# Kernel tuning notes

Measured on AMD Instinct MI355X. Metric: run time of the kernel, lower is better.

Reference implementation:

```python
import jax, jax.numpy as jnp
import numpy as np

B, N, R, E = 4, 50000, 100000, 1_600_000   # batch, nodes (wavelets_col), wavelets_row, nnz
D_IN, H1, H2, D_OUT = 32, 32, 16, 1
NEG_SLOPE = 0.2


def _xavier(k, shape):
    lim = float(np.sqrt(6.0 / (shape[0] + shape[1])))
    return jax.random.uniform(k, shape, jnp.float32, -lim, lim)


def setup_inputs() -> dict:
    key = jax.random.key(0)
    ks = jax.random.split(key, 16)
    # wavelets: sparse (R x N); inverse wavelets: sparse (N x R)
    w_rows = jax.random.randint(ks[0], (E,), 0, R)
    w_cols = jax.random.randint(ks[1], (E,), 0, N)
    wi_rows = jax.random.randint(ks[2], (E,), 0, N)
    wi_cols = jax.random.randint(ks[3], (E,), 0, R)
    return {
        "wavelets_indices": jnp.stack([w_rows, w_cols]),
        "wavelets_values": jax.random.normal(ks[4], (E,), jnp.float32) * 0.05,
        "wavelets_inverse_indices": jnp.stack([wi_rows, wi_cols]),
        "wavelets_inverse_values": jax.random.normal(ks[5], (E,), jnp.float32) * 0.05,
        "x_features": jax.random.normal(ks[6], (B, N, D_IN), jnp.float32),
        "W1": _xavier(ks[7], (D_IN, H1)),
        "diag1": 0.9 + 0.2 * jax.random.uniform(ks[8], (R,), jnp.float32),
        "W2": _xavier(ks[9], (H1, H2)),
        "diag2": 0.9 + 0.2 * jax.random.uniform(ks[10], (R,), jnp.float32),
        "reg_co_w": _xavier(ks[11], (H2, D_OUT)),
        "reg_co_b": jnp.zeros((D_OUT,), jnp.float32),
        "reg_co2_w": _xavier(ks[12], (H2, D_OUT)),
        "reg_co2_b": jnp.zeros((D_OUT,), jnp.float32),
    }


def _gw_layer(x, W, diag, w_idx, w_val, wi_idx, wi_val):
    # filtered = X @ W  -> (B, N, d)
    h = jnp.einsum("bnd,de->bne", x, W)
    d = W.shape[1]
    # T = wavelets (R x N) @ h  : scatter-add of gathered edge messages
    msg = h[:, w_idx[1], :] * w_val[None, :, None]          # (B, E, d)
    t = jnp.zeros((x.shape[0], R, d), h.dtype).at[:, w_idx[0], :].add(msg)
    # out = (wavelets_inverse * diag) (N x R) @ T  (diag rescales columns)
    coef = wi_val * diag[wi_idx[1]]                         # (E,)
    msg2 = t[:, wi_idx[1], :] * coef[None, :, None]         # (B, E, d)
    out = jnp.zeros((x.shape[0], N, d), h.dtype).at[:, wi_idx[0], :].add(msg2)
    return jax.nn.leaky_relu(out, NEG_SLOPE)                # dropout p=0.0 -> identity


def reference(wavelets_indices, wavelets_values, wavelets_inverse_indices,
              wavelets_inverse_values, x_features, W1, diag1, W2, diag2,
              reg_co_w, reg_co_b, reg_co2_w, reg_co2_b):
    x = _gw_layer(x_features, W1, diag1, wavelets_indices, wavelets_values,
                  wavelets_inverse_indices, wavelets_inverse_values)
    x = _gw_layer(x, W2, diag2, wavelets_indices, wavelets_values,
                  wavelets_inverse_indices, wavelets_inverse_values)
    co = x[:, -2, :] @ reg_co_w + reg_co_b                  # (B, 1)
    co2 = x[:, -1, :] @ reg_co2_w + reg_co2_b               # (B, 1)
    return jnp.concatenate([co[:, None, :], co2[:, None, :]], axis=1)  # (B, 2, 1)
```

## Files before the change

kernel.cpp:

```cpp
#include <hip/hip_runtime.h>

#define NEG_SLOPE 0.2f

static const int B = 4, N = 50000, R = 100000, E = 1600000;
static const int X2_CAP = 4096;
static const int R2_CAP = 4096;
static const int N1_CAP = 4096;
static const int WDEG  = 64;
static const int WIDEG = 96;
static const int RBW = 3200;
static const int NBW = 1600;


__global__ void fusedA(const float* __restrict__ x, const float* __restrict__ W1,
                       float* __restrict__ h1,
                       const int4* __restrict__ wi_rows4, const int* __restrict__ wi_cols,
                       const float* __restrict__ wi_val,
                       unsigned* __restrict__ bitsR1, int2* __restrict__ x2list,
                       int* __restrict__ x2tail, int* __restrict__ r2list,
                       int* __restrict__ r2tail, int e4, int G1) {
    if ((int)blockIdx.x < G1) {
        __shared__ float sW[32 * 32];
        for (int i = threadIdx.x; i < 1024; i += blockDim.x) sW[i] = W1[i];
        __syncthreads();
        int id = blockIdx.x * blockDim.x + threadIdx.x;
        if (id >= N * B) return;
        int n = id >> 2, b = id & 3;
        const float* xr = x + ((size_t)b * N + n) * 32;
        float acc[32];
#pragma unroll
        for (int c = 0; c < 32; ++c) acc[c] = 0.f;
#pragma unroll
        for (int k = 0; k < 32; ++k) {
            float xv = xr[k];
#pragma unroll
            for (int c = 0; c < 32; ++c) acc[c] += xv * sW[k * 32 + c];
        }
        float* o = h1 + ((size_t)n * B + b) * 32;
#pragma unroll
        for (int c = 0; c < 32; ++c) o[c] = acc[c];
    } else {
        int blk = blockIdx.x - G1;
        int base = blk * (blockDim.x * 4) + threadIdx.x;
#pragma unroll
        for (int k = 0; k < 4; ++k) {
            int i = base + k * blockDim.x;
            if (i >= e4) continue;
            int4 r = wi_rows4[i];
            int rr[4] = {r.x, r.y, r.z, r.w};
#pragma unroll
            for (int j = 0; j < 4; ++j) {
                if (rr[j] >= N - 2) {
                    int ed = i * 4 + j;
                    int col = wi_cols[ed];
                    unsigned old = atomicOr(&bitsR1[col >> 5], 1u << (col & 31));
                    if (!((old >> (col & 31)) & 1u)) {
                        int p = atomicAdd(r2tail, 1);
                        if (p < R2_CAP) r2list[p] = col;
                    }
                    int pos = atomicAdd(x2tail, 1);
                    if (pos < X2_CAP)
                        x2list[pos] = make_int2(col * 2 + (rr[j] - (N - 2)),
                                                __float_as_int(wi_val[ed]));
                }
            }
        }
    }
}

__global__ void markB(const int4* __restrict__ w_rows4, const int* __restrict__ w_cols,
                      const unsigned* __restrict__ bitsR1, unsigned* __restrict__ bitsN1,
                      int* __restrict__ n1list, int* __restrict__ n1slot,
                      int* __restrict__ n1tail, int e4) {
    __shared__ int lcount, gbase;
    __shared__ int sbuf[1024];
    if (threadIdx.x == 0) lcount = 0;
    __syncthreads();
    int lane = threadIdx.x & 63;
    int i = blockIdx.x * blockDim.x + threadIdx.x;
    int4 r = make_int4(-1, -1, -1, -1);
    if (i < e4) r = w_rows4[i];
    int rr[4] = {r.x, r.y, r.z, r.w};
    unsigned fb[4];
#pragma unroll
    for (int j = 0; j < 4; ++j)
        fb[j] = (rr[j] >= 0) ? ((bitsR1[rr[j] >> 5] >> (rr[j] & 31)) & 1u) : 0u;
#pragma unroll
    for (int j = 0; j < 4; ++j) {
        bool isnew = false;
        int c = 0;
        if (fb[j]) {
            c = w_cols[i * 4 + j];
            unsigned old = atomicOr(&bitsN1[c >> 5], 1u << (c & 31));
            isnew = ((old >> (c & 31)) & 1u) == 0u;
        }
        unsigned long long m = __ballot(isnew);
        if (m) {
            int leader = __ffsll(m) - 1;
            int b0 = 0;
            if (lane == leader) b0 = atomicAdd(&lcount, __popcll(m));
            b0 = __shfl(b0, leader);
            if (isnew) sbuf[b0 + __popcll(m & ((1ull << lane) - 1))] = c;
        }
    }
    __syncthreads();
    if (threadIdx.x == 0) gbase = atomicAdd(n1tail, lcount);
    __syncthreads();
    for (int t = threadIdx.x; t < lcount; t += blockDim.x) {
        int n = sbuf[t];
        int slot = gbase + t;
        n1list[slot] = n;
        n1slot[n] = slot;
    }
}

__global__ void markC_wi(const int4* __restrict__ wi_rows4, const int* __restrict__ wi_cols,
                         const float* __restrict__ wi_val, const float* __restrict__ diag1,
                         const unsigned* __restrict__ bitsN1, const int* __restrict__ n1slot,
                         unsigned* __restrict__ bitsR2, int* __restrict__ wi_cnt,
                         int2* __restrict__ wi_pairsD,
                         int* __restrict__ r1list, int* __restrict__ r1tail, int e4) {
    __shared__ int lcount2, gbase2;
    __shared__ int r1buf[1024];
    if (threadIdx.x == 0) lcount2 = 0;
    __syncthreads();
    int lane = threadIdx.x & 63;
    int i = blockIdx.x * blockDim.x + threadIdx.x;
    int4 r = make_int4(-1, -1, -1, -1);
    if (i < e4) r = wi_rows4[i];
    int rr[4] = {r.x, r.y, r.z, r.w};
    unsigned fb[4];
#pragma unroll
    for (int j = 0; j < 4; ++j)
        fb[j] = (rr[j] >= 0) ? ((bitsN1[rr[j] >> 5] >> (rr[j] & 31)) & 1u) : 0u;
#pragma unroll
    for (int j = 0; j < 4; ++j) {
        bool isnew = false;
        int col = 0;
        if (fb[j]) {
            int ed = i * 4 + j;
            col = wi_cols[ed];
            float cf = wi_val[ed] * diag1[col];
            int slot = n1slot[rr[j]];
            int pos = atomicAdd(&wi_cnt[rr[j]], 1);
            if (slot < N1_CAP && pos < WIDEG)
                wi_pairsD[(size_t)slot * WIDEG + pos] =
                    make_int2(col, __float_as_int(cf));
            unsigned old = atomicOr(&bitsR2[col >> 5], 1u << (col & 31));
            isnew = ((old >> (col & 31)) & 1u) == 0u;
        }
        unsigned long long m2 = __ballot(isnew);
        if (m2) {
            int leader = __ffsll(m2) - 1;
            int b0 = 0;
            if (lane == leader) b0 = atomicAdd(&lcount2, __popcll(m2));
            b0 = __shfl(b0, leader);
            if (isnew)
                r1buf[b0 + __popcll(m2 & ((1ull << lane) - 1))] = col;
        }
    }
    __syncthreads();
    if (threadIdx.x == 0) gbase2 = atomicAdd(r1tail, lcount2);
    __syncthreads();
    for (int t = threadIdx.x; t < lcount2; t += blockDim.x) r1list[gbase2 + t] = r1buf[t];
}

__global__ void wplace(const int4* __restrict__ w_rows4, const int4* __restrict__ w_cols4,
                       const float4* __restrict__ w_val4,
                       const unsigned* __restrict__ bitsR1, const unsigned* __restrict__ bitsR2,
                       int* __restrict__ w_cnt, int2* __restrict__ w_pairsD, int e4) {
    int i = blockIdx.x * blockDim.x + threadIdx.x;
    if (i >= e4) return;
    int4 r = w_rows4[i];
    int4 c = w_cols4[i];
    float4 v = w_val4[i];
    int rr[4] = {r.x, r.y, r.z, r.w};
    int cc[4] = {c.x, c.y, c.z, c.w};
    float vv[4] = {v.x, v.y, v.z, v.w};
    unsigned fl[4];
#pragma unroll
    for (int j = 0; j < 4; ++j)
        fl[j] = ((bitsR1[rr[j] >> 5] | bitsR2[rr[j] >> 5]) >> (rr[j] & 31)) & 1u;
#pragma unroll
    for (int j = 0; j < 4; ++j) {
        if (fl[j]) {
            int pos = atomicAdd(&w_cnt[rr[j]], 1);
            if (pos < WDEG)
                w_pairsD[(size_t)rr[j] * WDEG + pos] =
                    make_int2(cc[j], __float_as_int(vv[j]));
        }
    }
}

__global__ void gather_t1(const float* __restrict__ h1, float* __restrict__ t1,
                          const int* __restrict__ w_cnt, const int2* __restrict__ w_pairsD,
                          const int* __restrict__ r1list, const int* __restrict__ r1tail) {
    int total = (*r1tail) * 32;
    int gstride = gridDim.x * blockDim.x;
    for (int idx = blockIdx.x * blockDim.x + threadIdx.x; idx < total; idx += gstride) {
        int row = r1list[idx >> 5];
        int rem = idx & 31;
        int c4 = rem & 7;
        int b = rem >> 3;
        int L = w_cnt[row]; if (L > WDEG) L = WDEG;
        const int2* pr = w_pairsD + (size_t)row * WDEG;
        const float4* sb = (const float4*)h1 + b * 8 + c4;
        float4 acc = make_float4(0.f, 0.f, 0.f, 0.f);
        int i = 0;
        int L4 = L & ~3;
        for (; i < L4; i += 4) {
            int2 p0 = pr[i + 0];
            int2 p1 = pr[i + 1];
            int2 p2 = pr[i + 2];
            int2 p3 = pr[i + 3];
            float4 s0 = sb[(size_t)p0.x * 32];
            float4 s1 = sb[(size_t)p1.x * 32];
            float4 s2 = sb[(size_t)p2.x * 32];
            float4 s3 = sb[(size_t)p3.x * 32];
            float v0 = __int_as_float(p0.y), v1 = __int_as_float(p1.y);
            float v2 = __int_as_float(p2.y), v3 = __int_as_float(p3.y);
            acc.x += v0 * s0.x + v1 * s1.x + v2 * s2.x + v3 * s3.x;
            acc.y += v0 * s0.y + v1 * s1.y + v2 * s2.y + v3 * s3.y;
            acc.z += v0 * s0.z + v1 * s1.z + v2 * s2.z + v3 * s3.z;
            acc.w += v0 * s0.w + v1 * s1.w + v2 * s2.w + v3 * s3.w;
        }
        for (; i < L; ++i) {
            int2 p = pr[i];
            float4 sv = sb[(size_t)p.x * 32];
            float v = __int_as_float(p.y);
            acc.x += v * sv.x; acc.y += v * sv.y; acc.z += v * sv.z; acc.w += v * sv.w;
        }
        ((float4*)t1)[(size_t)row * 32 + b * 8 + c4] = acc;
    }
}

__global__ void x1gemm2(const float* __restrict__ t1, const float* __restrict__ W2,
                        float* __restrict__ h2,
                        const int* __restrict__ n1list, const int* __restrict__ wi_cnt,
                        const int2* __restrict__ wi_pairsD,
                        const int* __restrict__ n1tail) {
    __shared__ float sW[32 * 16];
    __shared__ float xls[8][128];
    for (int i = threadIdx.x; i < 512; i += blockDim.x) sW[i] = W2[i];
    int n1c = *n1tail; if (n1c > N1_CAP) n1c = N1_CAP;
    int g = threadIdx.x >> 5;
    int t32 = threadIdx.x & 31;
    int b = t32 >> 3, c4 = t32 & 7;
    for (int base = blockIdx.x * 8; base < n1c; base += gridDim.x * 8) {
        int s = base + g;
        bool active = (s < n1c);
        int n = 0;
        if (active) {
            n = n1list[s];
            int L = wi_cnt[n]; if (L > WIDEG) L = WIDEG;
            const int2* pr = wi_pairsD + (size_t)s * WIDEG;
            const float4* sb = (const float4*)t1 + b * 8 + c4;
            float4 acc = make_float4(0.f, 0.f, 0.f, 0.f);
            int i = 0;
            int L2 = L & ~1;
            for (; i < L2; i += 2) {
                int2 p0 = pr[i + 0];
                int2 p1 = pr[i + 1];
                float4 s0 = sb[(size_t)p0.x * 32];
                float4 s1 = sb[(size_t)p1.x * 32];
                float v0 = __int_as_float(p0.y), v1 = __int_as_float(p1.y);
                acc.x += v0 * s0.x + v1 * s1.x;
                acc.y += v0 * s0.y + v1 * s1.y;
                acc.z += v0 * s0.z + v1 * s1.z;
                acc.w += v0 * s0.w + v1 * s1.w;
            }
            if (i < L) {
                int2 p = pr[i];
                float4 sv = sb[(size_t)p.x * 32];
                float v = __int_as_float(p.y);
                acc.x += v * sv.x; acc.y += v * sv.y; acc.z += v * sv.z; acc.w += v * sv.w;
            }
            float* xp = &xls[g][b * 32 + c4 * 4];
            xp[0] = acc.x > 0.f ? acc.x : NEG_SLOPE * acc.x;
            xp[1] = acc.y > 0.f ? acc.y : NEG_SLOPE * acc.y;
            xp[2] = acc.z > 0.f ? acc.z : NEG_SLOPE * acc.z;
            xp[3] = acc.w > 0.f ? acc.w : NEG_SLOPE * acc.w;
        }
        __syncthreads();
        if (active) {
#pragma unroll
            for (int half = 0; half < 2; ++half) {
                int o = t32 + half * 32;
                int bb = o >> 4, cc = o & 15;
                const float* xp = &xls[g][bb * 32];
                float acc = 0.f;
#pragma unroll
                for (int k = 0; k < 32; ++k) acc += xp[k] * sW[k * 16 + cc];
                h2[(size_t)n * 64 + o] = acc;
            }
        }
        __syncthreads();
    }
}

__global__ void t2x2heads(const float* __restrict__ h2,
                          const int* __restrict__ w_cnt, const int2* __restrict__ w_pairsD,
                          const int* __restrict__ r2list, const int* __restrict__ r2tail,
                          float* __restrict__ t2,
                          const int2* __restrict__ x2list, const int* __restrict__ x2tail,
                          const float* __restrict__ diag2,
                          const float* __restrict__ rw1, const float* __restrict__ rb1,
                          const float* __restrict__ rw2, const float* __restrict__ rb2,
                          float* __restrict__ out) {
    int r2c = *r2tail; if (r2c > R2_CAP) r2c = R2_CAP;
    for (int idx = threadIdx.x; idx < r2c * 16; idx += blockDim.x) {
        int row = r2list[idx >> 4];
        int rem = idx & 15;
        int c4 = rem & 3;
        int b = rem >> 2;
        int L = w_cnt[row]; if (L > WDEG) L = WDEG;
        const int2* pr = w_pairsD + (size_t)row * WDEG;
        const float4* sb = (const float4*)h2 + b * 4 + c4;
        float4 acc = make_float4(0.f, 0.f, 0.f, 0.f);
        for (int i = 0; i < L; ++i) {
            int2 p = pr[i];
            float4 sv = sb[(size_t)p.x * 16];
            float v = __int_as_float(p.y);
            acc.x += v * sv.x; acc.y += v * sv.y; acc.z += v * sv.z; acc.w += v * sv.w;
        }
        ((float4*)t2)[(size_t)row * 16 + b * 4 + c4] = acc;
    }
    __syncthreads();

    int cnt = *x2tail; if (cnt > X2_CAP) cnt = X2_CAP;
    int g = threadIdx.x >> 6, l = threadIdx.x & 63;
    int b = l >> 4, c = l & 15;
    float a0 = 0.f, a1 = 0.f;
    for (int i = g; i < cnt; i += 16) {
        int2 rec = x2list[i];
        int col = rec.x >> 1;
        float coef = __int_as_float(rec.y) * diag2[col];
        float v = t2[(size_t)col * 64 + b * 16 + c] * coef;
        if (rec.x & 1) a1 += v; else a0 += v;
    }
    __shared__ float red0[16][64], red1[16][64], xs[2][64];
    red0[g][l] = a0; red1[g][l] = a1;
    __syncthreads();
    if (threadIdx.x < 64) {
        float s0 = 0.f, s1 = 0.f;
#pragma unroll
        for (int gg = 0; gg < 16; ++gg) { s0 += red0[gg][l]; s1 += red1[gg][l]; }
        xs[0][l] = s0; xs[1][l] = s1;
    }
    __syncthreads();
    if (threadIdx.x < 8) {
        int bb = threadIdx.x >> 1, which = threadIdx.x & 1;
        const float* w = which ? rw2 : rw1;
        float acc = which ? rb2[0] : rb1[0];
        for (int k = 0; k < 16; ++k) {
            float xv = xs[which][bb * 16 + k];
            xv = xv > 0.f ? xv : NEG_SLOPE * xv;
            acc += xv * w[k];
        }
        out[bb * 2 + which] = acc;
    }
}

extern "C" void kernel_launch(void* const* d_in, const int* in_sizes, int n_in,
                              void* d_out, int out_size, void* d_ws, size_t ws_size,
                              hipStream_t stream) {
    const int*   w_rows  = (const int*)d_in[0];
    const int*   w_cols  = ((const int*)d_in[0]) + E;
    const float* w_val   = (const float*)d_in[1];
    const int*   wi_rows = (const int*)d_in[2];
    const int*   wi_cols = ((const int*)d_in[2]) + E;
    const float* wi_val  = (const float*)d_in[3];
    const float* x       = (const float*)d_in[4];
    const float* W1      = (const float*)d_in[5];
    const float* diag1   = (const float*)d_in[6];
    const float* W2      = (const float*)d_in[7];
    const float* diag2   = (const float*)d_in[8];
    const float* rw1     = (const float*)d_in[9];
    const float* rb1     = (const float*)d_in[10];
    const float* rw2     = (const float*)d_in[11];
    const float* rb2     = (const float*)d_in[12];
    float* out = (float*)d_out;

    float* h1 = (float*)d_ws;
    float* t1 = h1 + (size_t)B * N * 32;
    float* h2 = t1 + (size_t)B * R * 32;
    int* ip = (int*)(h2 + (size_t)B * N * 16);
    int* w_cnt  = ip; ip += R;
    int* wi_cnt = ip; ip += N;
    unsigned* bitsR1 = (unsigned*)ip; ip += RBW;
    unsigned* bitsR2 = (unsigned*)ip; ip += RBW;
    unsigned* bitsN1 = (unsigned*)ip; ip += NBW;
    int* tails  = ip; ip += 8;
    size_t zero_words = (size_t)(ip - w_cnt);
    int*  n1slot = ip; ip += N;
    int*  n1list = ip; ip += N;
    int*  r1list = ip; ip += R;
    int*  r2list = ip; ip += R2_CAP;
    int2* x2list = (int2*)ip; ip += 2 * X2_CAP;
    int2* w_pairsD  = (int2*)ip; ip += 2 * (size_t)R * WDEG;
    int2* wi_pairsD = (int2*)ip; ip += 2 * (size_t)N1_CAP * WIDEG;

    float* t2 = t1;

    const int blk = 256;
    const int e4 = E / 4;
    const int G1 = (N * B + blk - 1) / blk;
    const int G2 = (e4 + blk * 4 - 1) / (blk * 4);
    const int scanGrid = (e4 + blk - 1) / blk;

    (void)hipMemsetAsync(w_cnt, 0, zero_words * sizeof(int), stream);

    fusedA<<<G1 + G2, blk, 0, stream>>>(x, W1, h1, (const int4*)wi_rows, wi_cols, wi_val,
                                        bitsR1, x2list, tails + 0, r2list, tails + 1,
                                        e4, G1);
    markB<<<scanGrid, blk, 0, stream>>>((const int4*)w_rows, w_cols, bitsR1, bitsN1,
                                        n1list, n1slot, tails + 2, e4);
    markC_wi<<<scanGrid, blk, 0, stream>>>((const int4*)wi_rows, wi_cols, wi_val, diag1,
                                           bitsN1, n1slot, bitsR2, wi_cnt, wi_pairsD,
                                           r1list, tails + 3, e4);
    wplace<<<scanGrid, blk, 0, stream>>>((const int4*)w_rows, (const int4*)w_cols,
                                         (const float4*)w_val, bitsR1, bitsR2,
                                         w_cnt, w_pairsD, e4);
    gather_t1<<<4096, blk, 0, stream>>>(h1, t1, w_cnt, w_pairsD, r1list, tails + 3);
    x1gemm2<<<256, blk, 0, stream>>>(t1, W2, h2, n1list, wi_cnt, wi_pairsD, tails + 2);
    t2x2heads<<<1, 1024, 0, stream>>>(h2, w_cnt, w_pairsD, r2list, tails + 1,
                                      t2, x2list, tails + 0, diag2,
                                      rw1, rb1, rw2, rb2, out);
}
```

Measured before the change: 278.1 us.

## Build full CSR for both matrices and fuse layer-1 into per-node gather MLP

Replaces the multi-pass marking pipeline (fusedA/markB/markC_wi/wplace/gather_t1/x1gemm2) with a single build kernel that buckets every edge of both sparse matrices by row, a small kernel that derives the needed node set from the final rows, and a fused kernel. The fused kernel aggregates raw x through the two sparse hops, then applies W1, leaky ReLU and W2 per needed node. It relies on linearity to move the W1 projection after aggregation, so no full h1 or t1 is materialized. In exchange it writes full bucket lists for all edges with unconditional atomics and recomputes the inner t rows per (node, edge).

```diff
diff --git a/kernel.cpp b/kernel.cpp
--- a/kernel.cpp
+++ b/kernel.cpp
@@ -10,289 +10,170 @@
 static const int WIDEG = 96;
 static const int RBW = 3200;
 static const int NBW = 1600;
-
-
-__global__ void fusedA(const float* __restrict__ x, const float* __restrict__ W1,
-                       float* __restrict__ h1,
-                       const int4* __restrict__ wi_rows4, const int* __restrict__ wi_cols,
-                       const float* __restrict__ wi_val,
-                       unsigned* __restrict__ bitsR1, int2* __restrict__ x2list,
-                       int* __restrict__ x2tail, int* __restrict__ r2list,
-                       int* __restrict__ r2tail, int e4, int G1) {
-    if ((int)blockIdx.x < G1) {
-        __shared__ float sW[32 * 32];
-        for (int i = threadIdx.x; i < 1024; i += blockDim.x) sW[i] = W1[i];
-        __syncthreads();
-        int id = blockIdx.x * blockDim.x + threadIdx.x;
-        if (id >= N * B) return;
-        int n = id >> 2, b = id & 3;
-        const float* xr = x + ((size_t)b * N + n) * 32;
-        float acc[32];
-#pragma unroll
-        for (int c = 0; c < 32; ++c) acc[c] = 0.f;
-#pragma unroll
-        for (int k = 0; k < 32; ++k) {
-            float xv = xr[k];
-#pragma unroll
-            for (int c = 0; c < 32; ++c) acc[c] += xv * sW[k * 32 + c];
-        }
-        float* o = h1 + ((size_t)n * B + b) * 32;
-#pragma unroll
-        for (int c = 0; c < 32; ++c) o[c] = acc[c];
-    } else {
-        int blk = blockIdx.x - G1;
-        int base = blk * (blockDim.x * 4) + threadIdx.x;
-#pragma unroll
-        for (int k = 0; k < 4; ++k) {
-            int i = base + k * blockDim.x;
-            if (i >= e4) continue;
-            int4 r = wi_rows4[i];
-            int rr[4] = {r.x, r.y, r.z, r.w};
-#pragma unroll
-            for (int j = 0; j < 4; ++j) {
-                if (rr[j] >= N - 2) {
-                    int ed = i * 4 + j;
-                    int col = wi_cols[ed];
-                    unsigned old = atomicOr(&bitsR1[col >> 5], 1u << (col & 31));
-                    if (!((old >> (col & 31)) & 1u)) {
-                        int p = atomicAdd(r2tail, 1);
-                        if (p < R2_CAP) r2list[p] = col;
-                    }
-                    int pos = atomicAdd(x2tail, 1);
-                    if (pos < X2_CAP)
-                        x2list[pos] = make_int2(col * 2 + (rr[j] - (N - 2)),
-                                                __float_as_int(wi_val[ed]));
+static const int ZWORDS = R + N + RBW + NBW + 8;
+
+
+__global__ void buildK(const int4* __restrict__ w_rows4, const int4* __restrict__ w_cols4,
+                       const float4* __restrict__ w_val4,
+                       const int4* __restrict__ wi_rows4, const int4* __restrict__ wi_cols4,
+                       const float4* __restrict__ wi_val4,
+                       int* __restrict__ w_cnt, int2* __restrict__ w_pairsD,
+                       int* __restrict__ wi_cnt, int2* __restrict__ wi_pairsD,
+                       unsigned* __restrict__ bitsR2d, int* __restrict__ r2list,
+                       int2* __restrict__ x2list, int* __restrict__ tails, int e4) {
+    int i = blockIdx.x * blockDim.x + threadIdx.x;
+    if (i < e4) {
+        int4 r = w_rows4[i];
+        int4 c = w_cols4[i];
+        float4 v = w_val4[i];
+        int rr[4] = {r.x, r.y, r.z, r.w};
+        int cc[4] = {c.x, c.y, c.z, c.w};
+        float vv[4] = {v.x, v.y, v.z, v.w};
+        int pos[4];
+#pragma unroll
+        for (int j = 0; j < 4; ++j) pos[j] = atomicAdd(&w_cnt[rr[j]], 1);
+#pragma unroll
+        for (int j = 0; j < 4; ++j)
+            if (pos[j] < WDEG)
+                w_pairsD[(size_t)rr[j] * WDEG + pos[j]] =
+                    make_int2(cc[j], __float_as_int(vv[j]));
+    } else if (i < 2 * e4) {
+        int k = i - e4;
+        int4 r = wi_rows4[k];
+        int4 c = wi_cols4[k];
+        float4 v = wi_val4[k];
+        int rr[4] = {r.x, r.y, r.z, r.w};
+        int cc[4] = {c.x, c.y, c.z, c.w};
+        float vv[4] = {v.x, v.y, v.z, v.w};
+        int pos[4];
+#pragma unroll
+        for (int j = 0; j < 4; ++j) pos[j] = atomicAdd(&wi_cnt[rr[j]], 1);
+#pragma unroll
+        for (int j = 0; j < 4; ++j)
+            if (pos[j] < WIDEG)
+                wi_pairsD[(size_t)rr[j] * WIDEG + pos[j]] =
+                    make_int2(cc[j], __float_as_int(vv[j]));
+#pragma unroll
+        for (int j = 0; j < 4; ++j) {
+            if (rr[j] >= N - 2) {
+                int col = cc[j];
+                unsigned old = atomicOr(&bitsR2d[col >> 5], 1u << (col & 31));
+                if (!((old >> (col & 31)) & 1u)) {
+                    int p = atomicAdd(&tails[1], 1);
+                    if (p < R2_CAP) r2list[p] = col;
                 }
-            }
-        }
-    }
-}
-
-__global__ void markB(const int4* __restrict__ w_rows4, const int* __restrict__ w_cols,
-                      const unsigned* __restrict__ bitsR1, unsigned* __restrict__ bitsN1,
-                      int* __restrict__ n1list, int* __restrict__ n1slot,
-                      int* __restrict__ n1tail, int e4) {
-    __shared__ int lcount, gbase;
-    __shared__ int sbuf[1024];
-    if (threadIdx.x == 0) lcount = 0;
-    __syncthreads();
-    int lane = threadIdx.x & 63;
-    int i = blockIdx.x * blockDim.x + threadIdx.x;
-    int4 r = make_int4(-1, -1, -1, -1);
-    if (i < e4) r = w_rows4[i];
-    int rr[4] = {r.x, r.y, r.z, r.w};
-    unsigned fb[4];
-#pragma unroll
-    for (int j = 0; j < 4; ++j)
-        fb[j] = (rr[j] >= 0) ? ((bitsR1[rr[j] >> 5] >> (rr[j] & 31)) & 1u) : 0u;
-#pragma unroll
-    for (int j = 0; j < 4; ++j) {
-        bool isnew = false;
-        int c = 0;
-        if (fb[j]) {
-            c = w_cols[i * 4 + j];
+                int q = atomicAdd(&tails[0], 1);
+                if (q < X2_CAP)
+                    x2list[q] = make_int2(col * 2 + (rr[j] - (N - 2)),
+                                          __float_as_int(vv[j]));
+            }
+        }
+    }
+}
+
+__global__ void n1build(const int* __restrict__ r2list,
+                        const int* __restrict__ w_cnt, const int2* __restrict__ w_pairsD,
+                        unsigned* __restrict__ bitsN1, int* __restrict__ n1list,
+                        int* __restrict__ tails) {
+    int r2c = tails[1]; if (r2c > R2_CAP) r2c = R2_CAP;
+    int total = r2c * WDEG;
+    for (int item = threadIdx.x; item < total; item += blockDim.x) {
+        int ri = item >> 6;
+        int e  = item & 63;
+        int row = r2list[ri];
+        int L = w_cnt[row]; if (L > WDEG) L = WDEG;
+        if (e < L) {
+            int c = w_pairsD[(size_t)row * WDEG + e].x;
             unsigned old = atomicOr(&bitsN1[c >> 5], 1u << (c & 31));
-            isnew = ((old >> (c & 31)) & 1u) == 0u;
-        }
-        unsigned long long m = __ballot(isnew);
-        if (m) {
-            int leader = __ffsll(m) - 1;
-            int b0 = 0;
-            if (lane == leader) b0 = atomicAdd(&lcount, __popcll(m));
-            b0 = __shfl(b0, leader);
-            if (isnew) sbuf[b0 + __popcll(m & ((1ull << lane) - 1))] = c;
-        }
-    }
-    __syncthreads();
-    if (threadIdx.x == 0) gbase = atomicAdd(n1tail, lcount);
-    __syncthreads();
-    for (int t = threadIdx.x; t < lcount; t += blockDim.x) {
-        int n = sbuf[t];
-        int slot = gbase + t;
-        n1list[slot] = n;
-        n1slot[n] = slot;
-    }
-}
-
-__global__ void markC_wi(const int4* __restrict__ wi_rows4, const int* __restrict__ wi_cols,
-                         const float* __restrict__ wi_val, const float* __restrict__ diag1,
-                         const unsigned* __restrict__ bitsN1, const int* __restrict__ n1slot,
-                         unsigned* __restrict__ bitsR2, int* __restrict__ wi_cnt,
-                         int2* __restrict__ wi_pairsD,
-                         int* __restrict__ r1list, int* __restrict__ r1tail, int e4) {
-    __shared__ int lcount2, gbase2;
-    __shared__ int r1buf[1024];
-    if (threadIdx.x == 0) lcount2 = 0;
-    __syncthreads();
-    int lane = threadIdx.x & 63;
-    int i = blockIdx.x * blockDim.x + threadIdx.x;
-    int4 r = make_int4(-1, -1, -1, -1);
-    if (i < e4) r = wi_rows4[i];
-    int rr[4] = {r.x, r.y, r.z, r.w};
-    unsigned fb[4];
-#pragma unroll
-    for (int j = 0; j < 4; ++j)
-        fb[j] = (rr[j] >= 0) ? ((bitsN1[rr[j] >> 5] >> (rr[j] & 31)) & 1u) : 0u;
-#pragma unroll
-    for (int j = 0; j < 4; ++j) {
-        bool isnew = false;
-        int col = 0;
-        if (fb[j]) {
-            int ed = i * 4 + j;
-            col = wi_cols[ed];
-            float cf = wi_val[ed] * diag1[col];
-            int slot = n1slot[rr[j]];
-            int pos = atomicAdd(&wi_cnt[rr[j]], 1);
-            if (slot < N1_CAP && pos < WIDEG)
-                wi_pairsD[(size_t)slot * WIDEG + pos] =
-                    make_int2(col, __float_as_int(cf));
-            unsigned old = atomicOr(&bitsR2[col >> 5], 1u << (col & 31));
-            isnew = ((old >> (col & 31)) & 1u) == 0u;
-        }
-        unsigned long long m2 = __ballot(isnew);
-        if (m2) {
-            int leader = __ffsll(m2) - 1;
-            int b0 = 0;
-            if (lane == leader) b0 = atomicAdd(&lcount2, __popcll(m2));
-            b0 = __shfl(b0, leader);
-            if (isnew)
-                r1buf[b0 + __popcll(m2 & ((1ull << lane) - 1))] = col;
-        }
-    }
-    __syncthreads();
-    if (threadIdx.x == 0) gbase2 = atomicAdd(r1tail, lcount2);
-    __syncthreads();
-    for (int t = threadIdx.x; t < lcount2; t += blockDim.x) r1list[gbase2 + t] = r1buf[t];
-}
-
-__global__ void wplace(const int4* __restrict__ w_rows4, const int4* __restrict__ w_cols4,
-                       const float4* __restrict__ w_val4,
-                       const unsigned* __restrict__ bitsR1, const unsigned* __restrict__ bitsR2,
-                       int* __restrict__ w_cnt, int2* __restrict__ w_pairsD, int e4) {
-    int i = blockIdx.x * blockDim.x + threadIdx.x;
-    if (i >= e4) return;
-    int4 r = w_rows4[i];
-    int4 c = w_cols4[i];
-    float4 v = w_val4[i];
-    int rr[4] = {r.x, r.y, r.z, r.w};
-    int cc[4] = {c.x, c.y, c.z, c.w};
-    float vv[4] = {v.x, v.y, v.z, v.w};
-    unsigned fl[4];
-#pragma unroll
-    for (int j = 0; j < 4; ++j)
-        fl[j] = ((bitsR1[rr[j] >> 5] | bitsR2[rr[j] >> 5]) >> (rr[j] & 31)) & 1u;
-#pragma unroll
-    for (int j = 0; j < 4; ++j) {
-        if (fl[j]) {
-            int pos = atomicAdd(&w_cnt[rr[j]], 1);
-            if (pos < WDEG)
-                w_pairsD[(size_t)rr[j] * WDEG + pos] =
-                    make_int2(cc[j], __float_as_int(vv[j]));
-        }
-    }
-}
-
-__global__ void gather_t1(const float* __restrict__ h1, float* __restrict__ t1,
-                          const int* __restrict__ w_cnt, const int2* __restrict__ w_pairsD,
-                          const int* __restrict__ r1list, const int* __restrict__ r1tail) {
-    int total = (*r1tail) * 32;
-    int gstride = gridDim.x * blockDim.x;
-    for (int idx = blockIdx.x * blockDim.x + threadIdx.x; idx < total; idx += gstride) {
-        int row = r1list[idx >> 5];
-        int rem = idx & 31;
-        int c4 = rem & 7;
-        int b = rem >> 3;
-        int L = w_cnt[row]; if (L > WDEG) L = WDEG;
-        const int2* pr = w_pairsD + (size_t)row * WDEG;
-        const float4* sb = (const float4*)h1 + b * 8 + c4;
+            if (!((old >> (c & 31)) & 1u)) {
+                int p = atomicAdd(&tails[2], 1);
+                if (p < N1_CAP) n1list[p] = c;
+            }
+        }
+    }
+}
+
+__global__ void __launch_bounds__(256) x1mlp(
+        const float* __restrict__ x, const float* __restrict__ diag1,
+        const float* __restrict__ W1, const float* __restrict__ W2,
+        const int* __restrict__ n1list, const int* __restrict__ tails,
+        const int* __restrict__ wi_cnt, const int2* __restrict__ wi_pairsD,
+        const int* __restrict__ w_cnt, const int2* __restrict__ w_pairsD,
+        float* __restrict__ h2) {
+    __shared__ float W1s[1024], W2s[512];
+    __shared__ float uls[8][128];
+    __shared__ float ufin[128], x1ls[128];
+    for (int i = threadIdx.x; i < 1024; i += 256) W1s[i] = W1[i];
+    for (int i = threadIdx.x; i < 512; i += 256) W2s[i] = W2[i];
+    int n1c = tails[2]; if (n1c > N1_CAP) n1c = N1_CAP;
+    int g = threadIdx.x >> 5, t32 = threadIdx.x & 31;
+    int b = t32 >> 3, c4 = t32 & 7;
+    const float4* xb = (const float4*)x + (size_t)b * N * 8 + c4;
+    for (int s = blockIdx.x; s < n1c; s += gridDim.x) {
+        int n = n1list[s];
+        int L = wi_cnt[n]; if (L > WIDEG) L = WIDEG;
+        const int2* wip = wi_pairsD + (size_t)n * WIDEG;
         float4 acc = make_float4(0.f, 0.f, 0.f, 0.f);
-        int i = 0;
-        int L4 = L & ~3;
-        for (; i < L4; i += 4) {
-            int2 p0 = pr[i + 0];
-            int2 p1 = pr[i + 1];
-            int2 p2 = pr[i + 2];
-            int2 p3 = pr[i + 3];
-            float4 s0 = sb[(size_t)p0.x * 32];
-            float4 s1 = sb[(size_t)p1.x * 32];
-            float4 s2 = sb[(size_t)p2.x * 32];
-            float4 s3 = sb[(size_t)p3.x * 32];
-            float v0 = __int_as_float(p0.y), v1 = __int_as_float(p1.y);
-            float v2 = __int_as_float(p2.y), v3 = __int_as_float(p3.y);
-            acc.x += v0 * s0.x + v1 * s1.x + v2 * s2.x + v3 * s3.x;
-            acc.y += v0 * s0.y + v1 * s1.y + v2 * s2.y + v3 * s3.y;
-            acc.z += v0 * s0.z + v1 * s1.z + v2 * s2.z + v3 * s3.z;
-            acc.w += v0 * s0.w + v1 * s1.w + v2 * s2.w + v3 * s3.w;
-        }
-        for (; i < L; ++i) {
-            int2 p = pr[i];
-            float4 sv = sb[(size_t)p.x * 32];
-            float v = __int_as_float(p.y);
-            acc.x += v * sv.x; acc.y += v * sv.y; acc.z += v * sv.z; acc.w += v * sv.w;
-        }
-        ((float4*)t1)[(size_t)row * 32 + b * 8 + c4] = acc;
-    }
-}
-
-__global__ void x1gemm2(const float* __restrict__ t1, const float* __restrict__ W2,
-                        float* __restrict__ h2,
-                        const int* __restrict__ n1list, const int* __restrict__ wi_cnt,
-                        const int2* __restrict__ wi_pairsD,
-                        const int* __restrict__ n1tail) {
-    __shared__ float sW[32 * 16];
-    __shared__ float xls[8][128];
-    for (int i = threadIdx.x; i < 512; i += blockDim.x) sW[i] = W2[i];
-    int n1c = *n1tail; if (n1c > N1_CAP) n1c = N1_CAP;
-    int g = threadIdx.x >> 5;
-    int t32 = threadIdx.x & 31;
-    int b = t32 >> 3, c4 = t32 & 7;
-    for (int base = blockIdx.x * 8; base < n1c; base += gridDim.x * 8) {
-        int s = base + g;
-        bool active = (s < n1c);
-        int n = 0;
-        if (active) {
-            n = n1list[s];
-            int L = wi_cnt[n]; if (L > WIDEG) L = WIDEG;
-            const int2* pr = wi_pairsD + (size_t)s * WIDEG;
-            const float4* sb = (const float4*)t1 + b * 8 + c4;
-            float4 acc = make_float4(0.f, 0.f, 0.f, 0.f);
+        for (int e = g; e < L; e += 8) {
+            int2 pe = wip[e];
+            int r = pe.x;
+            float coef = __int_as_float(pe.y) * diag1[r];
+            int Lw = w_cnt[r]; if (Lw > WDEG) Lw = WDEG;
+            const int2* pr = w_pairsD + (size_t)r * WDEG;
+            float4 t = make_float4(0.f, 0.f, 0.f, 0.f);
             int i = 0;
-            int L2 = L & ~1;
-            for (; i < L2; i += 2) {
+            int L4 = Lw & ~3;
+            for (; i < L4; i += 4) {
                 int2 p0 = pr[i + 0];
                 int2 p1 = pr[i + 1];
-                float4 s0 = sb[(size_t)p0.x * 32];
-                float4 s1 = sb[(size_t)p1.x * 32];
+                int2 p2 = pr[i + 2];
+                int2 p3 = pr[i + 3];
+                float4 s0 = xb[(size_t)p0.x * 8];
+                float4 s1 = xb[(size_t)p1.x * 8];
+                float4 s2 = xb[(size_t)p2.x * 8];
+                float4 s3 = xb[(size_t)p3.x * 8];
                 float v0 = __int_as_float(p0.y), v1 = __int_as_float(p1.y);
-                acc.x += v0 * s0.x + v1 * s1.x;
-                acc.y += v0 * s0.y + v1 * s1.y;
-                acc.z += v0 * s0.z + v1 * s1.z;
-                acc.w += v0 * s0.w + v1 * s1.w;
-            }
-            if (i < L) {
+                float v2 = __int_as_float(p2.y), v3 = __int_as_float(p3.y);
+                t.x += v0 * s0.x + v1 * s1.x + v2 * s2.x + v3 * s3.x;
+                t.y += v0 * s0.y + v1 * s1.y + v2 * s2.y + v3 * s3.y;
+                t.z += v0 * s0.z + v1 * s1.z + v2 * s2.z + v3 * s3.z;
+                t.w += v0 * s0.w + v1 * s1.w + v2 * s2.w + v3 * s3.w;
+            }
+            for (; i < Lw; ++i) {
                 int2 p = pr[i];
-                float4 sv = sb[(size_t)p.x * 32];
+                float4 sv = xb[(size_t)p.x * 8];
                 float v = __int_as_float(p.y);
-                acc.x += v * sv.x; acc.y += v * sv.y; acc.z += v * sv.z; acc.w += v * sv.w;
-            }
-            float* xp = &xls[g][b * 32 + c4 * 4];
-            xp[0] = acc.x > 0.f ? acc.x : NEG_SLOPE * acc.x;
-            xp[1] = acc.y > 0.f ? acc.y : NEG_SLOPE * acc.y;
-            xp[2] = acc.z > 0.f ? acc.z : NEG_SLOPE * acc.z;
-            xp[3] = acc.w > 0.f ? acc.w : NEG_SLOPE * acc.w;
-        }
-        __syncthreads();
-        if (active) {
-#pragma unroll
-            for (int half = 0; half < 2; ++half) {
-                int o = t32 + half * 32;
-                int bb = o >> 4, cc = o & 15;
-                const float* xp = &xls[g][bb * 32];
-                float acc = 0.f;
-#pragma unroll
-                for (int k = 0; k < 32; ++k) acc += xp[k] * sW[k * 16 + cc];
-                h2[(size_t)n * 64 + o] = acc;
-            }
+                t.x += v * sv.x; t.y += v * sv.y; t.z += v * sv.z; t.w += v * sv.w;
+            }
+            acc.x += coef * t.x; acc.y += coef * t.y;
+            acc.z += coef * t.z; acc.w += coef * t.w;
+        }
+        float* up = &uls[g][b * 32 + c4 * 4];
+        up[0] = acc.x; up[1] = acc.y; up[2] = acc.z; up[3] = acc.w;
+        __syncthreads();
+        if (threadIdx.x < 128) {
+            float sum = 0.f;
+#pragma unroll
+            for (int gg = 0; gg < 8; ++gg) sum += uls[gg][threadIdx.x];
+            ufin[threadIdx.x] = sum;
+        }
+        __syncthreads();
+        if (threadIdx.x < 128) {
+            int bb = threadIdx.x >> 5, c = threadIdx.x & 31;
+            const float* ur = &ufin[bb * 32];
+            float o = 0.f;
+#pragma unroll
+            for (int k = 0; k < 32; ++k) o += ur[k] * W1s[k * 32 + c];
+            x1ls[threadIdx.x] = o > 0.f ? o : NEG_SLOPE * o;
+        }
+        __syncthreads();
+        if (threadIdx.x < 64) {
+            int bb = threadIdx.x >> 4, c = threadIdx.x & 15;
+            const float* xr = &x1ls[bb * 32];
+            float o = 0.f;
+#pragma unroll
+            for (int k = 0; k < 32; ++k) o += xr[k] * W2s[k * 16 + c];
+            h2[(size_t)n * 64 + bb * 16 + c] = o;
         }
         __syncthreads();
     }
@@ -300,14 +181,14 @@
 
 __global__ void t2x2heads(const float* __restrict__ h2,
                           const int* __restrict__ w_cnt, const int2* __restrict__ w_pairsD,
-                          const int* __restrict__ r2list, const int* __restrict__ r2tail,
+                          const int* __restrict__ r2list, const int* __restrict__ tails,
                           float* __restrict__ t2,
-                          const int2* __restrict__ x2list, const int* __restrict__ x2tail,
+                          const int2* __restrict__ x2list,
                           const float* __restrict__ diag2,
                           const float* __restrict__ rw1, const float* __restrict__ rb1,
                           const float* __restrict__ rw2, const float* __restrict__ rb2,
                           float* __restrict__ out) {
-    int r2c = *r2tail; if (r2c > R2_CAP) r2c = R2_CAP;
+    int r2c = tails[1]; if (r2c > R2_CAP) r2c = R2_CAP;
     for (int idx = threadIdx.x; idx < r2c * 16; idx += blockDim.x) {
         int row = r2list[idx >> 4];
         int rem = idx & 15;
@@ -327,7 +208,7 @@
     }
     __syncthreads();
 
-    int cnt = *x2tail; if (cnt > X2_CAP) cnt = X2_CAP;
+    int cnt = tails[0]; if (cnt > X2_CAP) cnt = X2_CAP;
     int g = threadIdx.x >> 6, l = threadIdx.x & 63;
     int b = l >> 4, c = l & 15;
     float a0 = 0.f, a1 = 0.f;
@@ -344,8 +225,8 @@
     if (threadIdx.x < 64) {
         float s0 = 0.f, s1 = 0.f;
 #pragma unroll
-        for (int gg = 0; gg < 16; ++gg) { s0 += red0[gg][l]; s1 += red1[gg][l]; }
-        xs[0][l] = s0; xs[1][l] = s1;
+        for (int gg = 0; gg < 16; ++gg) { s0 += red0[gg][threadIdx.x]; s1 += red1[gg][threadIdx.x]; }
+        xs[0][threadIdx.x] = s0; xs[1][threadIdx.x] = s1;
     }
     __syncthreads();
     if (threadIdx.x < 8) {
@@ -381,49 +262,35 @@
     const float* rb2     = (const float*)d_in[12];
     float* out = (float*)d_out;
 
-    float* h1 = (float*)d_ws;
-    float* t1 = h1 + (size_t)B * N * 32;
-    float* h2 = t1 + (size_t)B * R * 32;
-    int* ip = (int*)(h2 + (size_t)B * N * 16);
+    float* h2 = (float*)d_ws;
+    float* t2 = h2 + (size_t)B * N * 16;
+    int* ip = (int*)(t2 + (size_t)B * R * 16);
     int* w_cnt  = ip; ip += R;
     int* wi_cnt = ip; ip += N;
-    unsigned* bitsR1 = (unsigned*)ip; ip += RBW;
-    unsigned* bitsR2 = (unsigned*)ip; ip += RBW;
-    unsigned* bitsN1 = (unsigned*)ip; ip += NBW;
-    int* tails  = ip; ip += 8;
-    size_t zero_words = (size_t)(ip - w_cnt);
-    int*  n1slot = ip; ip += N;
-    int*  n1list = ip; ip += N;
-    int*  r1list = ip; ip += R;
-    int*  r2list = ip; ip += R2_CAP;
+    unsigned* bitsR2d = (unsigned*)ip; ip += RBW;
+    unsigned* bitsN1  = (unsigned*)ip; ip += NBW;
+    int* tails = ip; ip += 8;
+    int* n1list = ip; ip += N1_CAP;
+    int* r2list = ip; ip += R2_CAP;
     int2* x2list = (int2*)ip; ip += 2 * X2_CAP;
     int2* w_pairsD  = (int2*)ip; ip += 2 * (size_t)R * WDEG;
-    int2* wi_pairsD = (int2*)ip; ip += 2 * (size_t)N1_CAP * WIDEG;
-
-    float* t2 = t1;
-
-    const int blk = 256;
+    int2* wi_pairsD = (int2*)ip; ip += 2 * (size_t)N * WIDEG;
+
     const int e4 = E / 4;
-    const int G1 = (N * B + blk - 1) / blk;
-    const int G2 = (e4 + blk * 4 - 1) / (blk * 4);
-    const int scanGrid = (e4 + blk - 1) / blk;
-
-    (void)hipMemsetAsync(w_cnt, 0, zero_words * sizeof(int), stream);
-
-    fusedA<<<G1 + G2, blk, 0, stream>>>(x, W1, h1, (const int4*)wi_rows, wi_cols, wi_val,
-                                        bitsR1, x2list, tails + 0, r2list, tails + 1,
-                                        e4, G1);
-    markB<<<scanGrid, blk, 0, stream>>>((const int4*)w_rows, w_cols, bitsR1, bitsN1,
-                                        n1list, n1slot, tails + 2, e4);
-    markC_wi<<<scanGrid, blk, 0, stream>>>((const int4*)wi_rows, wi_cols, wi_val, diag1,
-                                           bitsN1, n1slot, bitsR2, wi_cnt, wi_pairsD,
-                                           r1list, tails + 3, e4);
-    wplace<<<scanGrid, blk, 0, stream>>>((const int4*)w_rows, (const int4*)w_cols,
-                                         (const float4*)w_val, bitsR1, bitsR2,
-                                         w_cnt, w_pairsD, e4);
-    gather_t1<<<4096, blk, 0, stream>>>(h1, t1, w_cnt, w_pairsD, r1list, tails + 3);
-    x1gemm2<<<256, blk, 0, stream>>>(t1, W2, h2, n1list, wi_cnt, wi_pairsD, tails + 2);
-    t2x2heads<<<1, 1024, 0, stream>>>(h2, w_cnt, w_pairsD, r2list, tails + 1,
-                                      t2, x2list, tails + 0, diag2,
-                                      rw1, rb1, rw2, rb2, out);
-}
+
+    (void)hipMemsetAsync(w_cnt, 0, (size_t)ZWORDS * sizeof(int), stream);
+
+    buildK<<<(2 * e4 + 255) / 256, 256, 0, stream>>>(
+        (const int4*)w_rows, (const int4*)w_cols, (const float4*)w_val,
+        (const int4*)wi_rows, (const int4*)wi_cols, (const float4*)wi_val,
+        w_cnt, w_pairsD, wi_cnt, wi_pairsD,
+        bitsR2d, r2list, x2list, tails, e4);
+
+    n1build<<<1, 256, 0, stream>>>(r2list, w_cnt, w_pairsD, bitsN1, n1list, tails);
+
+    x1mlp<<<1024, 256, 0, stream>>>(x, diag1, W1, W2, n1list, tails,
+                                    wi_cnt, wi_pairsD, w_cnt, w_pairsD, h2);
+
+    t2x2heads<<<1, 1024, 0, stream>>>(h2, w_cnt, w_pairsD, r2list, tails,
+                                      t2, x2list, diag2, rw1, rb1, rw2, rb2, out);
+}
```

Result: slower. 452.8 us (+62.8%).
